# Optimization experiments

Hardware: AMD Instinct MI355X
Metric: run time of the kernel (lower is better)

## Reference

```python
import jax, jax.numpy as jnp
import numpy as np

TEMPERATURE = 5.0

def setup_inputs() -> dict:
    key = jax.random.key(0)
    k1, k2 = jax.random.split(key)
    B, D = 8192, 128
    features = jax.random.normal(k1, (B, D), dtype=jnp.float32)
    labels = jax.random.randint(k2, (B,), 0, 100, dtype=jnp.int64)
    return {"features": features, "labels": labels, "fac_label": 3}


def reference(features, labels, fac_label):
    # features: [B, D], labels: [B]
    B = features.shape[0]
    # positive-pair mask; note original's mask_scale row-copy loop is a no-op,
    # so mask_scale == mask, and mask_cross_feature == ones (fac_label unused in effect)
    mask = (labels[:, None] == labels[None, :]).astype(features.dtype)  # [B, B]

    sim = jnp.matmul(features, features.T) / TEMPERATURE  # [B, B]
    logits_max = jax.lax.stop_gradient(jnp.max(sim, axis=1, keepdims=True))
    logits = sim - logits_max

    # remove self-contrast (diagonal)
    logits_mask = 1.0 - jnp.eye(B, dtype=features.dtype)
    mask = mask * logits_mask

    exp_logits = jnp.exp(logits) * logits_mask
    log_prob = logits - jnp.log(1e-12 + exp_logits.sum(axis=1, keepdims=True))

    mean_log_prob_pos_mask = (mask * log_prob).sum(axis=1)  # [B]
    # vectorized form of the per-element reciprocal loop: 1/count where count>0 else 0
    cnt = mask.sum(axis=1)
    recip = jnp.where(cnt == 0, 0.0, 1.0 / jnp.where(cnt == 0, 1.0, cnt))

    loss = -(mean_log_prob_pos_mask * recip).mean()
    return loss
```

## Files before the change

### kernel.cpp

```cpp
#include <hip/hip_runtime.h>


#define BN 8192
#define DK 128
#define INV_T 0.2f
#define C1F 0.28853901f
#define C40F 27.7258872f

#define CHUNKS 32
#define CCOLS (BN / CHUNKS)
#define RPB 256
#define RT 4
#define NJT (CCOLS / 16)

#define NCLS 100
#define PB 128
#define PROWS (BN / PB)

#define OFF_FB    0
#define OFF_PART  (2 * 1024 * 1024)
#define OFF_GP    (OFF_PART + 2 * 1024 * 1024)
#define OFF_HISTP (OFF_GP + PB * NCLS * DK * 4)
#define OFF_G     (OFF_HISTP + PB * NCLS * 4)
#define OFF_HIST  (OFF_G + NCLS * DK * 4)
#define OFF_BSUM  (OFF_HIST + 512)
#define OFF_CTR   (OFF_BSUM + 256)

typedef __attribute__((ext_vector_type(8))) short bf16x8;
typedef __attribute__((ext_vector_type(4))) float f32x4;

#define FENCE() asm volatile("" ::: "memory")

__device__ __forceinline__ unsigned short f2bf(float f) {
    unsigned u = __builtin_bit_cast(unsigned, f);
    u += 0x7fffu + ((u >> 16) & 1u);
    return (unsigned short)(u >> 16);
}

__device__ __forceinline__ float fexp2(float x) {
#if __has_builtin(__builtin_amdgcn_exp2f)
    return __builtin_amdgcn_exp2f(x);
#else
    float r; asm("v_exp_f32 %0, %1" : "=v"(r) : "v"(x)); return r;
#endif
}

__device__ __forceinline__ void load_lds16(const void* g, void* l) {
    __builtin_amdgcn_global_load_lds(
        (const __attribute__((address_space(1))) unsigned int*)g,
        (__attribute__((address_space(3))) unsigned int*)l, 16, 0, 0);
}

__global__ __launch_bounds__(256) void prep_kernel(const float* __restrict__ F,
                                                   const int* __restrict__ labels,
                                                   unsigned short* __restrict__ Fb,
                                                   float* __restrict__ Gp,
                                                   int* __restrict__ histp,
                                                   unsigned int* __restrict__ ctr) {
    const int t  = threadIdx.x;
    const int b  = blockIdx.x;
    const int r0 = b * PROWS;

    if (b == 0 && t == 0) *ctr = 0u;

    const float4* F4  = (const float4*)F + (size_t)b * (PROWS * DK / 4);
    ushort4*      Fb4 = (ushort4*)Fb + (size_t)b * (PROWS * DK / 4);
#pragma unroll
    for (int k = 0; k < PROWS * DK / 4 / 256; ++k) {
        float4 v = F4[k * 256 + t];
        ushort4 o;
        o.x = f2bf(v.x); o.y = f2bf(v.y); o.z = f2bf(v.z); o.w = f2bf(v.w);
        Fb4[k * 256 + t] = o;
    }

    __shared__ int   ll[PROWS];
    __shared__ int   lh[NCLS];
    __shared__ float gl[2][NCLS][DK];
    float4* gl4 = (float4*)gl;
    if (t < NCLS) lh[t] = 0;
    if (t < PROWS) ll[t] = labels[r0 + t];
#pragma unroll
    for (int k = 0; k < 2 * NCLS * DK / 4 / 256; ++k)
        gl4[k * 256 + t] = make_float4(0.f, 0.f, 0.f, 0.f);
    __syncthreads();

    if (t < PROWS) atomicAdd(&lh[ll[t]], 1);

    {
        const int half = t >> 7, col = t & 127;
        const int rb   = half * (PROWS / 2);
        for (int rr = 0; rr < PROWS / 2; ++rr) {
            const int lr = rb + rr;
            gl[half][ll[lr]][col] += F[(size_t)(r0 + lr) * DK + col];
        }
    }
    __syncthreads();

    if (t < NCLS) histp[b * NCLS + t] = lh[t];
    const float* gl0 = (const float*)gl;
#pragma unroll
    for (int k = 0; k < NCLS * DK / 256; ++k) {
        const int idx = k * 256 + t;
        Gp[(size_t)b * (NCLS * DK) + idx] = gl0[idx] + gl0[NCLS * DK + idx];
    }
}

template <bool DIAGBLK>
__device__ __forceinline__ void supcon_rows(const short* __restrict__ Fb,
                                            float2* __restrict__ part,
                                            int bx, int by, char* smem) {
    const int t    = threadIdx.x;
    const int wave = t >> 6, lane = t & 63;
    const int quad = lane >> 4, l16 = lane & 15;
    const int rowBase = bx * RPB + wave * (RT * 16);
    const int colBase = by * CCOLS;

    bf16x8 a[RT][4];
#pragma unroll
    for (int rt = 0; rt < RT; ++rt)
#pragma unroll
        for (int kt = 0; kt < 4; ++kt)
            a[rt][kt] = *(const bf16x8*)(Fb + (size_t)(rowBase + rt * 16 + l16) * DK
                                            + kt * 32 + quad * 8);

    float mr[RT][4], Zs[RT][4];
#pragma unroll
    for (int rt = 0; rt < RT; ++rt)
#pragma unroll
        for (int r = 0; r < 4; ++r) { mr[rt][r] = -__builtin_inff(); Zs[rt][r] = 0.f; }

    const int  L    = wave * 1024 + lane * 16;
    const int  sw   = (L & ~255) | ((L & 255) ^ ((L >> 4) & 0x70));
    const char* tile0 = (const char*)(Fb + (size_t)colBase * DK);
    char*       dst0  = smem + wave * 1024;

    int roff[4];
#pragma unroll
    for (int kt = 0; kt < 4; ++kt)
        roff[kt] = l16 * 256 + ((kt * 64 + quad * 16) ^ ((l16 & 7) << 4));

    auto STAGE = [&](int buf, int jt) {
        load_lds16(tile0 + (size_t)jt * 4096 + sw, dst0 + buf * 4096);
    };

    auto COMPUTE = [&](int buf, int jt) {
        bf16x8 bb[4];
#pragma unroll
        for (int kt = 0; kt < 4; ++kt)
            bb[kt] = *(const bf16x8*)(smem + buf * 4096 + roff[kt]);
        const int j0 = colBase + jt * 16;
#pragma unroll
        for (int rt = 0; rt < RT; ++rt) {
            f32x4 acc = {0.f, 0.f, 0.f, 0.f};
#pragma unroll
            for (int kt = 0; kt < 4; ++kt)
                acc = __builtin_amdgcn_mfma_f32_16x16x32_bf16(a[rt][kt], bb[kt], acc, 0, 0, 0);
#pragma unroll
            for (int r = 0; r < 4; ++r) {
                const float raw = acc[r];
                mr[rt][r] = fmaxf(mr[rt][r], raw);
                float e = fexp2(fmaf(raw, C1F, -40.0f));
                if (DIAGBLK) {
                    const int irow0 = rowBase + rt * 16 + quad * 4;
                    if (j0 + l16 == irow0 + r) e = 0.f;
                }
                Zs[rt][r] += e;
            }
        }
    };

    STAGE(0, 0); STAGE(1, 1); STAGE(2, 2);
    int jt = 0;
    for (; jt < NJT - 2; ++jt) {
        asm volatile("s_waitcnt vmcnt(2)" ::: "memory");
        __builtin_amdgcn_s_barrier();
        FENCE();
        COMPUTE(jt & 3, jt);
        FENCE();
        __builtin_amdgcn_s_barrier();
        FENCE();
        if (jt + 3 < NJT) STAGE((jt + 3) & 3, jt + 3);
    }
    asm volatile("s_waitcnt vmcnt(1)" ::: "memory");
    __builtin_amdgcn_s_barrier();
    FENCE();
    COMPUTE(jt & 3, jt);
    ++jt;
    asm volatile("s_waitcnt vmcnt(0)" ::: "memory");
    __builtin_amdgcn_s_barrier();
    FENCE();
    COMPUTE(jt & 3, jt);

#pragma unroll
    for (int rt = 0; rt < RT; ++rt)
#pragma unroll
        for (int r = 0; r < 4; ++r) {
            float mm = mr[rt][r], zz = Zs[rt][r];
#pragma unroll
            for (int h = 1; h < 16; h <<= 1) {
                mm = fmaxf(mm, __shfl_xor(mm, h));
                zz += __shfl_xor(zz, h);
            }
            if (l16 == 0)
                part[(size_t)by * BN + rowBase + rt * 16 + quad * 4 + r] =
                    make_float2(mm, zz);
        }
}

__global__ __launch_bounds__(256) void supcon_main(const short* __restrict__ Fb,
                                                   float2* __restrict__ part,
                                                   const float* __restrict__ Gp,
                                                   const int* __restrict__ histp,
                                                   float* __restrict__ G,
                                                   int* __restrict__ hist) {
    __shared__ alignas(16) char smem[16384];
    if (blockIdx.y == CHUNKS) {
        const int base = blockIdx.x * 256 + threadIdx.x;
        for (int idx = base; idx < NCLS * DK + NCLS; idx += BN) {
            if (idx < NCLS * DK) {
                float s = 0.f;
#pragma unroll 8
                for (int p = 0; p < PB; ++p) s += Gp[(size_t)p * (NCLS * DK) + idx];
                G[idx] = s;
            } else {
                const int c = idx - NCLS * DK;
                int s = 0;
#pragma unroll 8
                for (int p = 0; p < PB; ++p) s += histp[p * NCLS + c];
                hist[c] = s;
            }
        }
        return;
    }
    if (blockIdx.x == blockIdx.y) supcon_rows<true >(Fb, part, blockIdx.x, blockIdx.y, smem);
    else                          supcon_rows<false>(Fb, part, blockIdx.x, blockIdx.y, smem);
}

__global__ __launch_bounds__(256) void supcon_finalize(const float* __restrict__ F,
                                                       const int* __restrict__ labels,
                                                       const float2* __restrict__ part,
                                                       const float* __restrict__ G,
                                                       const int* __restrict__ hist,
                                                       float* __restrict__ bsums,
                                                       unsigned int* __restrict__ ctr,
                                                       float* __restrict__ out) {
    const int t = threadIdx.x;
    const int i = blockIdx.x * 256 + t;

    float mraw = -__builtin_inff(), Zm = 0.f;
#pragma unroll 8
    for (int c = 0; c < CHUNKS; ++c) {
        const float2 p = part[(size_t)c * BN + i];
        mraw = fmaxf(mraw, p.x);
        Zm += p.y;
    }
    const int   lbl = labels[i];
    const float cnt = (float)(hist[lbl] - 1);

    const float4* fr = (const float4*)(F + (size_t)i * DK);
    const float4* gr = (const float4*)(G + lbl * DK);
    float dot = 0.f, nrm = 0.f;
#pragma unroll 8
    for (int k = 0; k < DK / 4; ++k) {
        const float4 av = fr[k], gv = gr[k];
        dot += av.x * gv.x + av.y * gv.y + av.z * gv.z + av.w * gv.w;
        nrm += av.x * av.x + av.y * av.y + av.z * av.z + av.w * av.w;
    }

    const float m = mraw * INV_T;
    const float A = (dot - nrm) * INV_T;
    float term = 0.f;
    if (cnt > 0.5f)
        term = (A - cnt * m) / cnt - __logf(1e-12f + Zm * __expf(C40F - m));

    float sum = term;
#pragma unroll
    for (int h = 1; h < 64; h <<= 1) sum += __shfl_xor(sum, h);
    __shared__ float ss[4];
    if ((t & 63) == 0) ss[t >> 6] = sum;
    __syncthreads();
    if (t == 0) {
        bsums[blockIdx.x] = ss[0] + ss[1] + ss[2] + ss[3];
        __threadfence();
        const unsigned old = atomicAdd(ctr, 1u);
        if (old == (BN / 256) - 1) {
            __threadfence();
            float tot = 0.f;
            const volatile float* vb = bsums;
            for (int c = 0; c < BN / 256; ++c) tot += vb[c];
            out[0] = -tot * (1.0f / BN);
        }
    }
}

extern "C" void kernel_launch(void* const* d_in, const int* in_sizes, int n_in,
                              void* d_out, int out_size, void* d_ws, size_t ws_size,
                              hipStream_t stream) {
    const float* F      = (const float*)d_in[0];
    const int*   labels = (const int*)d_in[1];
    float* out = (float*)d_out;
    char*  ws  = (char*)d_ws;

    unsigned short* Fb    = (unsigned short*)(ws + OFF_FB);
    float2*         part  = (float2*)(ws + OFF_PART);
    float*          Gp    = (float*)(ws + OFF_GP);
    int*            histp = (int*)(ws + OFF_HISTP);
    float*          G     = (float*)(ws + OFF_G);
    int*            hist  = (int*)(ws + OFF_HIST);
    float*          bsums = (float*)(ws + OFF_BSUM);
    unsigned int*   ctr   = (unsigned int*)(ws + OFF_CTR);

    prep_kernel<<<PB, 256, 0, stream>>>(F, labels, Fb, Gp, histp, ctr);
    supcon_main<<<dim3(BN / RPB, CHUNKS + 1), 256, 0, stream>>>((const short*)Fb, part,
                                                                Gp, histp, G, hist);
    supcon_finalize<<<BN / 256, 256, 0, stream>>>(F, labels, part, G, hist,
                                                  bsums, ctr, out);
}
```

Baseline: 121.9 us.

## Exploit Gram symmetry: compute lower-triangular tiles and scatter row/column sums atomically

Since the similarity matrix is symmetric, only the lower triangle of 256x64 tiles is computed, and each tile's exp sums are added atomically to both its rows and its columns. The per-row max is replaced by the row's own squared norm, which is the diagonal of the Gram matrix. The partial buffers are zeroed in the prep kernel. This roughly halves the MFMA and exp work, at the cost of atomics, more and smaller blocks, and a change in how the bf16 max is chosen.

New measurement: 132.3 us. 1.09x slower.

```diff
diff --git a/kernel.cpp b/kernel.cpp
--- a/kernel.cpp
+++ b/kernel.cpp
@@ -7,11 +7,10 @@
 #define C1F 0.28853901f
 #define C40F 27.7258872f
 
-#define CHUNKS 32
-#define CCOLS (BN / CHUNKS)
-#define RPB 256
-#define RT 4
-#define NJT (CCOLS / 16)
+#define NBX    32
+#define TILES  2112
+#define RIDERS 32
+#define PSLOTS 32
 
 #define NCLS 100
 #define PB 128
@@ -19,7 +18,7 @@
 
 #define OFF_FB    0
 #define OFF_PART  (2 * 1024 * 1024)
-#define OFF_GP    (OFF_PART + 2 * 1024 * 1024)
+#define OFF_GP    (OFF_PART + PSLOTS * BN * 4)
 #define OFF_HISTP (OFF_GP + PB * NCLS * DK * 4)
 #define OFF_G     (OFF_HISTP + PB * NCLS * 4)
 #define OFF_HIST  (OFF_G + NCLS * DK * 4)
@@ -28,8 +27,6 @@
 
 typedef __attribute__((ext_vector_type(8))) short bf16x8;
 typedef __attribute__((ext_vector_type(4))) float f32x4;
-
-#define FENCE() asm volatile("" ::: "memory")
 
 __device__ __forceinline__ unsigned short f2bf(float f) {
     unsigned u = __builtin_bit_cast(unsigned, f);
@@ -54,6 +51,7 @@
 __global__ __launch_bounds__(256) void prep_kernel(const float* __restrict__ F,
                                                    const int* __restrict__ labels,
                                                    unsigned short* __restrict__ Fb,
+                                                   float* __restrict__ part,
                                                    float* __restrict__ Gp,
                                                    int* __restrict__ histp,
                                                    unsigned int* __restrict__ ctr) {
@@ -63,6 +61,13 @@
 
     if (b == 0 && t == 0) *ctr = 0u;
 
+    {
+        float4* pz = (float4*)part + (size_t)b * (PSLOTS * BN / 4 / PB);
+#pragma unroll
+        for (int k = 0; k < PSLOTS * BN / 4 / PB / 256; ++k)
+            pz[k * 256 + t] = make_float4(0.f, 0.f, 0.f, 0.f);
+    }
+
     const float4* F4  = (const float4*)F + (size_t)b * (PROWS * DK / 4);
     ushort4*      Fb4 = (ushort4*)Fb + (size_t)b * (PROWS * DK / 4);
 #pragma unroll
@@ -105,118 +110,99 @@
     }
 }
 
-template <bool DIAGBLK>
-__device__ __forceinline__ void supcon_rows(const short* __restrict__ Fb,
-                                            float2* __restrict__ part,
-                                            int bx, int by, char* smem) {
+template <bool DIAGT>
+__device__ __forceinline__ void supcon_tile(const short* __restrict__ Fb,
+                                            float* __restrict__ part,
+                                            int bx, int cy, char* smem) {
     const int t    = threadIdx.x;
     const int wave = t >> 6, lane = t & 63;
     const int quad = lane >> 4, l16 = lane & 15;
-    const int rowBase = bx * RPB + wave * (RT * 16);
-    const int colBase = by * CCOLS;
-
-    bf16x8 a[RT][4];
-#pragma unroll
-    for (int rt = 0; rt < RT; ++rt)
+    const int rowBase = bx * 256 + wave * 64;
+    const int colBase = cy * 64;
+
+    {
+        const char* Btile = (const char*)Fb + (size_t)colBase * 256;
+        const int   s     = wave * 64 + lane;
+        const int   gso   = (s & 15) * 256 + (s >> 6) * 64 + ((s >> 4) & 3) * 16;
+        char*       ldsw  = smem + wave * 1024;
+#pragma unroll
+        for (int jt = 0; jt < 4; ++jt)
+            load_lds16(Btile + jt * 4096 + gso, ldsw + jt * 4096);
+    }
+
+    bf16x8 a[4][4];
+#pragma unroll
+    for (int rt = 0; rt < 4; ++rt)
 #pragma unroll
         for (int kt = 0; kt < 4; ++kt)
             a[rt][kt] = *(const bf16x8*)(Fb + (size_t)(rowBase + rt * 16 + l16) * DK
                                             + kt * 32 + quad * 8);
 
-    float mr[RT][4], Zs[RT][4];
-#pragma unroll
-    for (int rt = 0; rt < RT; ++rt)
-#pragma unroll
-        for (int r = 0; r < 4; ++r) { mr[rt][r] = -__builtin_inff(); Zs[rt][r] = 0.f; }
-
-    const int  L    = wave * 1024 + lane * 16;
-    const int  sw   = (L & ~255) | ((L & 255) ^ ((L >> 4) & 0x70));
-    const char* tile0 = (const char*)(Fb + (size_t)colBase * DK);
-    char*       dst0  = smem + wave * 1024;
-
-    int roff[4];
-#pragma unroll
-    for (int kt = 0; kt < 4; ++kt)
-        roff[kt] = l16 * 256 + ((kt * 64 + quad * 16) ^ ((l16 & 7) << 4));
-
-    auto STAGE = [&](int buf, int jt) {
-        load_lds16(tile0 + (size_t)jt * 4096 + sw, dst0 + buf * 4096);
-    };
-
-    auto COMPUTE = [&](int buf, int jt) {
+    float Zs[4][4];
+#pragma unroll
+    for (int rt = 0; rt < 4; ++rt)
+#pragma unroll
+        for (int r = 0; r < 4; ++r) Zs[rt][r] = 0.f;
+
+    __syncthreads();
+
+    const int roffb = quad * 256 + l16 * 16;
+#pragma unroll
+    for (int jt = 0; jt < 4; ++jt) {
         bf16x8 bb[4];
 #pragma unroll
         for (int kt = 0; kt < 4; ++kt)
-            bb[kt] = *(const bf16x8*)(smem + buf * 4096 + roff[kt]);
-        const int j0 = colBase + jt * 16;
-#pragma unroll
-        for (int rt = 0; rt < RT; ++rt) {
+            bb[kt] = *(const bf16x8*)(smem + jt * 4096 + kt * 1024 + roffb);
+        float Zc = 0.f;
+#pragma unroll
+        for (int rt = 0; rt < 4; ++rt) {
             f32x4 acc = {0.f, 0.f, 0.f, 0.f};
 #pragma unroll
             for (int kt = 0; kt < 4; ++kt)
                 acc = __builtin_amdgcn_mfma_f32_16x16x32_bf16(a[rt][kt], bb[kt], acc, 0, 0, 0);
 #pragma unroll
             for (int r = 0; r < 4; ++r) {
-                const float raw = acc[r];
-                mr[rt][r] = fmaxf(mr[rt][r], raw);
-                float e = fexp2(fmaf(raw, C1F, -40.0f));
-                if (DIAGBLK) {
-                    const int irow0 = rowBase + rt * 16 + quad * 4;
-                    if (j0 + l16 == irow0 + r) e = 0.f;
+                float e = fexp2(fmaf(acc[r], C1F, -40.0f));
+                if (DIAGT) {
+                    if (colBase + jt * 16 + l16 == rowBase + rt * 16 + quad * 4 + r)
+                        e = 0.f;
                 }
                 Zs[rt][r] += e;
+                Zc       += e;
             }
         }
-    };
-
-    STAGE(0, 0); STAGE(1, 1); STAGE(2, 2);
-    int jt = 0;
-    for (; jt < NJT - 2; ++jt) {
-        asm volatile("s_waitcnt vmcnt(2)" ::: "memory");
-        __builtin_amdgcn_s_barrier();
-        FENCE();
-        COMPUTE(jt & 3, jt);
-        FENCE();
-        __builtin_amdgcn_s_barrier();
-        FENCE();
-        if (jt + 3 < NJT) STAGE((jt + 3) & 3, jt + 3);
-    }
-    asm volatile("s_waitcnt vmcnt(1)" ::: "memory");
-    __builtin_amdgcn_s_barrier();
-    FENCE();
-    COMPUTE(jt & 3, jt);
-    ++jt;
-    asm volatile("s_waitcnt vmcnt(0)" ::: "memory");
-    __builtin_amdgcn_s_barrier();
-    FENCE();
-    COMPUTE(jt & 3, jt);
-
-#pragma unroll
-    for (int rt = 0; rt < RT; ++rt)
+        if (!DIAGT) {
+            Zc += __shfl_xor(Zc, 16);
+            Zc += __shfl_xor(Zc, 32);
+            if (quad == 0)
+                atomicAdd(&part[(size_t)bx * BN + colBase + jt * 16 + l16], Zc);
+        }
+    }
+
+    const int slot = cy >> 2;
+#pragma unroll
+    for (int rt = 0; rt < 4; ++rt)
 #pragma unroll
         for (int r = 0; r < 4; ++r) {
-            float mm = mr[rt][r], zz = Zs[rt][r];
-#pragma unroll
-            for (int h = 1; h < 16; h <<= 1) {
-                mm = fmaxf(mm, __shfl_xor(mm, h));
-                zz += __shfl_xor(zz, h);
-            }
+            float zz = Zs[rt][r];
+#pragma unroll
+            for (int h = 1; h < 16; h <<= 1) zz += __shfl_xor(zz, h);
             if (l16 == 0)
-                part[(size_t)by * BN + rowBase + rt * 16 + quad * 4 + r] =
-                    make_float2(mm, zz);
+                atomicAdd(&part[(size_t)slot * BN + rowBase + rt * 16 + quad * 4 + r], zz);
         }
 }
 
 __global__ __launch_bounds__(256) void supcon_main(const short* __restrict__ Fb,
-                                                   float2* __restrict__ part,
+                                                   float* __restrict__ part,
                                                    const float* __restrict__ Gp,
                                                    const int* __restrict__ histp,
                                                    float* __restrict__ G,
                                                    int* __restrict__ hist) {
     __shared__ alignas(16) char smem[16384];
-    if (blockIdx.y == CHUNKS) {
-        const int base = blockIdx.x * 256 + threadIdx.x;
-        for (int idx = base; idx < NCLS * DK + NCLS; idx += BN) {
+    const int bid = blockIdx.x;
+    if (bid >= TILES) {
+        const int base = (bid - TILES) * 256 + threadIdx.x;
+        for (int idx = base; idx < NCLS * DK + NCLS; idx += RIDERS * 256) {
             if (idx < NCLS * DK) {
                 float s = 0.f;
 #pragma unroll 8
@@ -232,13 +218,18 @@
         }
         return;
     }
-    if (blockIdx.x == blockIdx.y) supcon_rows<true >(Fb, part, blockIdx.x, blockIdx.y, smem);
-    else                          supcon_rows<false>(Fb, part, blockIdx.x, blockIdx.y, smem);
+    float sq = sqrtf(2.0f * (float)bid + 1.0f);
+    int bx = (int)((sq - 1.0f) * 0.5f);
+    while (2 * (bx + 1) * (bx + 2) <= bid) ++bx;
+    while (bx > 0 && 2 * bx * (bx + 1) > bid) --bx;
+    const int cy = bid - 2 * bx * (bx + 1);
+    if (cy >= 4 * bx) supcon_tile<true >(Fb, part, bx, cy, smem);
+    else              supcon_tile<false>(Fb, part, bx, cy, smem);
 }
 
 __global__ __launch_bounds__(256) void supcon_finalize(const float* __restrict__ F,
                                                        const int* __restrict__ labels,
-                                                       const float2* __restrict__ part,
+                                                       const float* __restrict__ part,
                                                        const float* __restrict__ G,
                                                        const int* __restrict__ hist,
                                                        float* __restrict__ bsums,
@@ -247,13 +238,10 @@
     const int t = threadIdx.x;
     const int i = blockIdx.x * 256 + t;
 
-    float mraw = -__builtin_inff(), Zm = 0.f;
+    float Zm = 0.f;
 #pragma unroll 8
-    for (int c = 0; c < CHUNKS; ++c) {
-        const float2 p = part[(size_t)c * BN + i];
-        mraw = fmaxf(mraw, p.x);
-        Zm += p.y;
-    }
+    for (int c = 0; c < PSLOTS; ++c) Zm += part[(size_t)c * BN + i];
+
     const int   lbl = labels[i];
     const float cnt = (float)(hist[lbl] - 1);
 
@@ -267,11 +255,11 @@
         nrm += av.x * av.x + av.y * av.y + av.z * av.z + av.w * av.w;
     }
 
-    const float m = mraw * INV_T;
-    const float A = (dot - nrm) * INV_T;
+    const float mt = nrm * INV_T;
+    const float A  = (dot - nrm) * INV_T;
     float term = 0.f;
     if (cnt > 0.5f)
-        term = (A - cnt * m) / cnt - __logf(1e-12f + Zm * __expf(C40F - m));
+        term = (A - cnt * mt) / cnt - __logf(1e-12f + Zm * __expf(C40F - mt));
 
     float sum = term;
 #pragma unroll
@@ -302,7 +290,7 @@
     char*  ws  = (char*)d_ws;
 
     unsigned short* Fb    = (unsigned short*)(ws + OFF_FB);
-    float2*         part  = (float2*)(ws + OFF_PART);
+    float*          part  = (float*)(ws + OFF_PART);
     float*          Gp    = (float*)(ws + OFF_GP);
     int*            histp = (int*)(ws + OFF_HISTP);
     float*          G     = (float*)(ws + OFF_G);
@@ -310,9 +298,9 @@
     float*          bsums = (float*)(ws + OFF_BSUM);
     unsigned int*   ctr   = (unsigned int*)(ws + OFF_CTR);
 
-    prep_kernel<<<PB, 256, 0, stream>>>(F, labels, Fb, Gp, histp, ctr);
-    supcon_main<<<dim3(BN / RPB, CHUNKS + 1), 256, 0, stream>>>((const short*)Fb, part,
-                                                                Gp, histp, G, hist);
+    prep_kernel<<<PB, 256, 0, stream>>>(F, labels, Fb, part, Gp, histp, ctr);
+    supcon_main<<<TILES + RIDERS, 256, 0, stream>>>((const short*)Fb, part,
+                                                    Gp, histp, G, hist);
     supcon_finalize<<<BN / 256, 256, 0, stream>>>(F, labels, part, G, hist,
                                                   bsums, ctr, out);
 }
```
